# Performance work log

Measured on AMD Instinct MI355X. Metric: run time of the kernel, lower is better.

The kernel has to match this reference:

```python
import jax, jax.numpy as jnp
import numpy as np
from jax import lax

B, N, R, L = 16, 256, 24, 32
MEAN_STOP_TIME_S = 60.0
AVG_TRANSFER_WAIT_TIME_S = 300.0
SYMMETRIC_ROUTES = True
INF = jnp.inf


def setup_inputs() -> dict:
    key = jax.random.key(0)
    k1, k2, k3 = jax.random.split(key, 3)
    drive_times = jax.random.uniform(k1, (B, N, N), jnp.float32) * 1000.0 + 30.0
    demand = jax.random.uniform(k2, (B, N, N), jnp.float32) * 10.0
    demand = demand * (1.0 - jnp.eye(N, dtype=jnp.float32))  # no self-demand
    batch_routes = jax.random.randint(k3, (B, R, L), 0, N, dtype=jnp.int32)
    return {"drive_times": drive_times, "demand": demand, "batch_routes": batch_routes}


def _route_edges_and_legs(routes, dtm):
    # routes: [B,R,L] node ids (no -1 padding in this setup); dtm: [B,N,N]
    b = jnp.arange(B)[:, None, None]
    sf, st = routes[:, :, :-1], routes[:, :, 1:]
    leg_fwd = dtm[b, sf, st] + MEAN_STOP_TIME_S            # [B,R,L-1]
    zero = jnp.zeros((B, R, 1), dtm.dtype)
    cum_f = jnp.concatenate([zero, jnp.cumsum(leg_fwd, -1)], -1)  # [B,R,L]
    tri = jnp.triu(jnp.ones((L, L), dtype=bool), 1)
    # ride time from stop position i to position j>i along the route
    t_f = jnp.where(tri, cum_f[:, :, None, :] - cum_f[:, :, :, None], INF)
    b4 = jnp.arange(B)[:, None, None, None]
    src = jnp.broadcast_to(routes[:, :, :, None], (B, R, L, L))
    dst = jnp.broadcast_to(routes[:, :, None, :], (B, R, L, L))
    edge = jnp.full((B, N, N), INF, dtm.dtype)
    edge = edge.at[b4, src, dst].min(t_f)
    leg_rev = None
    if SYMMETRIC_ROUTES:
        leg_rev = dtm[b, st, sf] + MEAN_STOP_TIME_S        # reverse-direction legs
        cum_r = jnp.concatenate([zero, jnp.cumsum(leg_rev, -1)], -1)
        t_r = jnp.where(tri, cum_r[:, :, None, :] - cum_r[:, :, :, None], INF)
        edge = edge.at[b4, dst, src].min(t_r)              # ride from s_j back to s_i
    return edge, leg_fwd, leg_rev


def _floyd_warshall(edge):
    # batched FW, also tracking hop count of shortest paths
    idx = jnp.arange(N)
    dist = edge.at[:, idx, idx].set(0.0)
    offdiag = ~jnp.eye(N, dtype=bool)
    hops = jnp.where(jnp.isfinite(dist) & offdiag, 1.0, 0.0)

    def body(carry, k):
        d, h = carry
        dc = lax.dynamic_slice_in_dim(d, k, 1, axis=2)  # [B,N,1]
        dr = lax.dynamic_slice_in_dim(d, k, 1, axis=1)  # [B,1,N]
        hc = lax.dynamic_slice_in_dim(h, k, 1, axis=2)
        hr = lax.dynamic_slice_in_dim(h, k, 1, axis=1)
        alt = dc + dr
        better = alt < d
        return (jnp.where(better, alt, d), jnp.where(better, hc + hr, h)), None

    (dist, hops), _ = lax.scan(body, (dist, hops), idx)
    return dist, hops


def reference(drive_times, demand, batch_routes):
    edge, leg_fwd, leg_rev = _route_edges_and_legs(batch_routes, drive_times)
    dist, hops = _floyd_warshall(edge)
    nopath = jnp.isinf(dist)
    path_lens = jnp.where(nopath, 0.0, hops + 1.0)  # n nodes on path (diag -> 1)
    transfers = jnp.where(path_lens == 0.0, 0.0, path_lens - 2.0)
    trip_times = jnp.where(nopath, 0.0, dist + transfers * AVG_TRANSFER_WAIT_TIME_S)
    total_demand_time = (demand * trip_times).sum((1, 2))
    total_transfers = (demand * transfers).sum((1, 2))
    unserved_demand = jnp.where(nopath, demand, 0.0).sum((1, 2))
    total_demand = demand.sum((1, 2))
    n_disconnected = (nopath & (demand > 0)).sum((1, 2))
    buckets = [jnp.where(transfers == float(ii), demand, 0.0).sum((1, 2)) for ii in range(3)]
    d_un = jnp.where(transfers > 2.0, demand, 0.0).sum((1, 2)) + unserved_demand
    trips_at_transfers = jnp.stack(buckets + [d_un], axis=1)  # [B,4]
    total_route_time = leg_fwd.sum((1, 2))
    if SYMMETRIC_ROUTES:
        total_route_time = total_route_time + leg_rev.sum((1, 2))
    return (total_demand_time, total_route_time, trips_at_transfers,
            total_demand, unserved_demand, total_transfers, trip_times,
            n_disconnected)
```

## Files before the change

### kernel.cpp

```cpp
#include <hip/hip_runtime.h>

#define BB 16
#define NL 256
#define RR 24
#define LL 32
#define NN (NL*NL)
#define BNN (BB*NN)
#define TT 64

#define O_TDT 0
#define O_RT  16
#define O_TAT 32
#define O_TD  96
#define O_UNS 112
#define O_TTR 128
#define O_TT  144
#define O_ND  1048720

#define HSC 9.3132257461547852e-10
#define H2  1073741824.0
#define HMASK 8191

#define RIDX(r, c2) (((r)<<6) + ((((c2) ^ ((r)&31)))<<1))
#define LDD(A, r, c2) (*(double2*)&A[RIDX((r),(c2))])

__global__ void k_routes(const float* __restrict__ dtm, const int* __restrict__ routes,
                         unsigned long long* __restrict__ dist, float* __restrict__ acc){
    int br = blockIdx.x; int b = br / RR, r = br % RR;
    int lane = threadIdx.x;
    int gid = br*64 + lane;
    if (gid < BB*NL){
        int bq = gid >> 8, n = gid & 255;
        ((double*)dist)[bq*NN + n*(NL+1)] = 0.0;
    }
    __shared__ int   s[LL];
    __shared__ float lf[LL], lr[LL], cf[LL], cr[LL];
    if (lane < LL) s[lane] = routes[(b*RR + r)*LL + lane];
    __syncthreads();
    if (lane < LL-1){
        int a0 = s[lane], a1 = s[lane+1];
        const float* dt = dtm + b*NN;
        lf[lane] = dt[a0*NL + a1] + 60.0f;
        lr[lane] = dt[a1*NL + a0] + 60.0f;
    }
    __syncthreads();
    if (lane == 0){
        float af = 0.f, ar2 = 0.f;
        cf[0] = 0.f; cr[0] = 0.f;
        for (int l = 0; l < LL-1; l++){
            af += lf[l]; ar2 += lr[l];
            cf[l+1] = af; cr[l+1] = ar2;
        }
        atomicAdd(&acc[b*16 + 1], af + ar2);
    }
    __syncthreads();
    for (int p = lane; p < LL*LL; p += 64){
        int i = p >> 5, j = p & 31;
        if (j > i){
            double vf = (double)(cf[j] - cf[i]) + HSC;
            double vr = (double)(cr[j] - cr[i]) + HSC;
            atomicMin(&dist[b*NN + s[i]*NL + s[j]], (unsigned long long)__double_as_longlong(vf));
            atomicMin(&dist[b*NN + s[j]*NL + s[i]], (unsigned long long)__double_as_longlong(vr));
        }
    }
}

template<bool FINAL>
__global__ __launch_bounds__(512, 2) void k_fw(
        const double* __restrict__ src, double* __restrict__ dst, int kb,
        const float* __restrict__ demand, float* __restrict__ out,
        float* __restrict__ acc){
    int b  = blockIdx.y;
    int m  = blockIdx.x;
    int ti = m >> 2, tj = m & 3;
    int t  = threadIdx.x;
    int w  = t >> 6, lane = t & 63;
    int kh = lane >> 5, sub = lane & 31;
    int cA = sub & 15, cB = cA + 16;
    int r0 = w*8 + (sub >> 4)*4;
    __shared__ __align__(16) double KD[4096];
    __shared__ __align__(16) double BD[4096];
    const double* Kg = src + b*NN + kb*TT*(NL+1);
    const double* Bg = src + b*NN + (kb*NL + tj)*TT;
    const double* Cg = src + b*NN + (ti*NL + kb)*TT;
    const double* Dg = src + b*NN + (ti*NL + tj)*TT;

    double2 c0r[4];
    #pragma unroll
    for (int u = 0; u < 4; u++){
        int fid = u*512 + t, row = fid >> 5, cc = fid & 31;
        c0r[u] = *(const double2*)(Cg + row*NL + cc*2);
    }
    double2 d0a[4], d0b[4];
    #pragma unroll
    for (int i = 0; i < 4; i++){
        d0a[i] = *(const double2*)(Dg + (r0+i)*NL + 2*cA);
        d0b[i] = *(const double2*)(Dg + (r0+i)*NL + 2*cB);
    }

    #pragma unroll
    for (int u = 0; u < 4; u++){
        int fid = u*512 + t, row = fid >> 5, cc = fid & 31;
        LDD(KD, row, cc) = *(const double2*)(Kg + row*NL + cc*2);
        LDD(BD, row, cc) = *(const double2*)(Bg + row*NL + cc*2);
    }
    __syncthreads();

    for (int skb = 0; skb < 4; skb++){
        int s0 = skb*16, sc2 = skb*8;
        if (t < 64){
            int i = t >> 2, jg = t & 3, rr = s0 + i, cbk = sc2 + jg*2;
            double2 m0 = LDD(KD, rr, cbk), m1 = LDD(KD, rr, cbk+1);
            double md4[4] = {m0.x, m0.y, m1.x, m1.y};
            #pragma unroll
            for (int k = 0; k < 16; k++){
                double rd[4];
                #pragma unroll
                for (int c = 0; c < 4; c++) rd[c] = __shfl(md4[c], (k<<2)|jg);
                double cd = __shfl(md4[k&3], (i<<2)|(k>>2));
                #pragma unroll
                for (int c = 0; c < 4; c++) md4[c] = fmin(md4[c], cd + rd[c]);
            }
            LDD(KD, rr, cbk)   = make_double2(md4[0], md4[1]);
            LDD(KD, rr, cbk+1) = make_double2(md4[2], md4[3]);
        }
        __syncthreads();
        {
            double sv[4], av[16];
            int pr, pcA, pcB;
            if (t < 256){ pr = s0 + (t >> 4); pcA = t & 15;            pcB = pcA + 16; }
            else        { int t2 = t - 256; pr = t2 >> 2; pcA = sc2 + (t2 & 3); pcB = pcA + 4; }
            double2 v0 = LDD(KD, pr, pcA), v1 = LDD(KD, pr, pcB);
            sv[0]=v0.x; sv[1]=v0.y; sv[2]=v1.x; sv[3]=v1.y;
            #pragma unroll
            for (int c = 0; c < 8; c++){
                double2 a2 = LDD(KD, pr, sc2 + c);
                av[2*c] = a2.x; av[2*c+1] = a2.y;
            }
            #pragma unroll
            for (int k = 0; k < 16; k++){
                double2 b0 = LDD(KD, s0+k, pcA), b1 = LDD(KD, s0+k, pcB);
                sv[0] = fmin(sv[0], av[k] + b0.x);
                sv[1] = fmin(sv[1], av[k] + b0.y);
                sv[2] = fmin(sv[2], av[k] + b1.x);
                sv[3] = fmin(sv[3], av[k] + b1.y);
            }
            __syncthreads();
            LDD(KD, pr, pcA) = make_double2(sv[0], sv[1]);
            LDD(KD, pr, pcB) = make_double2(sv[2], sv[3]);
        }
        __syncthreads();
        double dd[4][4];
        #pragma unroll
        for (int i = 0; i < 4; i++){
            double2 v0 = LDD(KD, r0+i, cA), v1 = LDD(KD, r0+i, cB);
            dd[i][0]=v0.x; dd[i][1]=v0.y; dd[i][2]=v1.x; dd[i][3]=v1.y;
        }
        #pragma unroll
        for (int q4 = 0; q4 < 2; q4++){
            int kc = sc2 + kh*4 + q4*2;
            int kr = s0 + kh*8 + q4*4;
            double a[4][4], bm[4][4];
            #pragma unroll
            for (int i = 0; i < 4; i++){
                double2 a0 = LDD(KD, r0+i, kc), a1 = LDD(KD, r0+i, kc+1);
                a[i][0]=a0.x; a[i][1]=a0.y; a[i][2]=a1.x; a[i][3]=a1.y;
            }
            #pragma unroll
            for (int q = 0; q < 4; q++){
                double2 b0 = LDD(KD, kr+q, cA), b1 = LDD(KD, kr+q, cB);
                bm[q][0]=b0.x; bm[q][1]=b0.y; bm[q][2]=b1.x; bm[q][3]=b1.y;
            }
            #pragma unroll
            for (int q = 0; q < 4; q++)
            #pragma unroll
            for (int i = 0; i < 4; i++)
            #pragma unroll
            for (int j = 0; j < 4; j++)
                dd[i][j] = fmin(dd[i][j], a[i][q] + bm[q][j]);
        }
        #pragma unroll
        for (int i = 0; i < 4; i++)
        #pragma unroll
        for (int j = 0; j < 4; j++)
            dd[i][j] = fmin(dd[i][j], __shfl_xor(dd[i][j], 32));
        __syncthreads();
        #pragma unroll
        for (int i = 0; i < 4; i++){
            LDD(KD, r0+i, cA) = make_double2(dd[i][0], dd[i][1]);
            LDD(KD, r0+i, cB) = make_double2(dd[i][2], dd[i][3]);
        }
        __syncthreads();
    }

    double nanv = __longlong_as_double(0x7FF07FF07FF07FF0LL);
    double md[4][4];
    #pragma unroll
    for (int i = 0; i < 4; i++)
    #pragma unroll
    for (int j = 0; j < 4; j++) md[i][j] = nanv;
    #pragma unroll 2
    for (int q4 = 0; q4 < 8; q4++){
        int kc = kh*16 + q4*2;
        int kr = kh*32 + q4*4;
        double a[4][4], bm[4][4];
        #pragma unroll
        for (int i = 0; i < 4; i++){
            double2 a0 = LDD(KD, r0+i, kc), a1 = LDD(KD, r0+i, kc+1);
            a[i][0]=a0.x; a[i][1]=a0.y; a[i][2]=a1.x; a[i][3]=a1.y;
        }
        #pragma unroll
        for (int q = 0; q < 4; q++){
            double2 b0 = LDD(BD, kr+q, cA), b1 = LDD(BD, kr+q, cB);
            bm[q][0]=b0.x; bm[q][1]=b0.y; bm[q][2]=b1.x; bm[q][3]=b1.y;
        }
        #pragma unroll
        for (int q = 0; q < 4; q++)
        #pragma unroll
        for (int i = 0; i < 4; i++)
        #pragma unroll
        for (int j = 0; j < 4; j++)
            md[i][j] = fmin(md[i][j], a[i][q] + bm[q][j]);
    }
    #pragma unroll
    for (int i = 0; i < 4; i++)
    #pragma unroll
    for (int j = 0; j < 4; j++)
        md[i][j] = fmin(md[i][j], __shfl_xor(md[i][j], 32));
    __syncthreads();
    #pragma unroll
    for (int i = 0; i < 4; i++){
        LDD(BD, r0+i, cA) = make_double2(md[i][0], md[i][1]);
        LDD(BD, r0+i, cB) = make_double2(md[i][2], md[i][3]);
    }
    #pragma unroll
    for (int u = 0; u < 4; u++){
        int fid = u*512 + t, row = fid >> 5, cc = fid & 31;
        LDD(KD, row, cc) = c0r[u];
    }
    __syncthreads();

    double dd[4][4];
    #pragma unroll
    for (int i = 0; i < 4; i++){
        dd[i][0]=d0a[i].x; dd[i][1]=d0a[i].y; dd[i][2]=d0b[i].x; dd[i][3]=d0b[i].y;
    }
    #pragma unroll 2
    for (int q4 = 0; q4 < 8; q4++){
        int kc = kh*16 + q4*2;
        int kr = kh*32 + q4*4;
        double a[4][4], bm[4][4];
        #pragma unroll
        for (int i = 0; i < 4; i++){
            double2 a0 = LDD(KD, r0+i, kc), a1 = LDD(KD, r0+i, kc+1);
            a[i][0]=a0.x; a[i][1]=a0.y; a[i][2]=a1.x; a[i][3]=a1.y;
        }
        #pragma unroll
        for (int q = 0; q < 4; q++){
            double2 b0 = LDD(BD, kr+q, cA), b1 = LDD(BD, kr+q, cB);
            bm[q][0]=b0.x; bm[q][1]=b0.y; bm[q][2]=b1.x; bm[q][3]=b1.y;
        }
        #pragma unroll
        for (int q = 0; q < 4; q++)
        #pragma unroll
        for (int i = 0; i < 4; i++)
        #pragma unroll
        for (int j = 0; j < 4; j++)
            dd[i][j] = fmin(dd[i][j], a[i][q] + bm[q][j]);
    }
    #pragma unroll
    for (int i = 0; i < 4; i++)
    #pragma unroll
    for (int j = 0; j < 4; j++)
        dd[i][j] = fmin(dd[i][j], __shfl_xor(dd[i][j], 32));

    if (!FINAL){
        if (kh == 0){
            double* Od = dst + b*NN + (ti*NL + tj)*TT;
            #pragma unroll
            for (int i = 0; i < 4; i++){
                *(double2*)(Od + (r0+i)*NL + 2*cA) = make_double2(dd[i][0], dd[i][1]);
                *(double2*)(Od + (r0+i)*NL + 2*cB) = make_double2(dd[i][2], dd[i][3]);
            }
        }
        return;
    }

    float s9[9];
    #pragma unroll
    for (int q = 0; q < 9; q++) s9[q] = 0.f;
    if (kh == 0){
        #pragma unroll
        for (int i = 0; i < 4; i++){
            const float* dmg = demand + b*NN + (ti*TT + r0 + i)*NL + tj*TT;
            float* ttg = out + O_TT + b*NN + (ti*TT + r0 + i)*NL + tj*TT;
            float2 m0 = *(const float2*)(dmg + 2*cA);
            float2 m1 = *(const float2*)(dmg + 2*cB);
            float dmv[4] = {m0.x, m0.y, m1.x, m1.y};
            float tts[4];
            #pragma unroll
            for (int e = 0; e < 4; e++){
                double v = dd[i][e];
                bool np = !(v < 1e37);
                double vv = np ? 0.0 : v;
                int h = (int)(((long long)(vv * H2)) & (long long)HMASK);
                float d = (float)vv;
                float dm = dmv[e];
                float pl = np ? 0.f : (float)(h + 1);
                float tr = (pl == 0.f) ? 0.f : pl - 2.f;
                float tt = np ? 0.f : d + tr*300.f;
                tts[e] = tt;
                s9[0] += dm*tt;
                s9[1] += dm*tr;
                s9[2] += np ? dm : 0.f;
                s9[3] += dm;
                s9[4] += (np && dm > 0.f) ? 1.f : 0.f;
                s9[5] += (tr == 0.f) ? dm : 0.f;
                s9[6] += (tr == 1.f) ? dm : 0.f;
                s9[7] += (tr == 2.f) ? dm : 0.f;
                s9[8] += (tr > 2.f) ? dm : 0.f;
            }
            *(float2*)(ttg + 2*cA) = make_float2(tts[0], tts[1]);
            *(float2*)(ttg + 2*cB) = make_float2(tts[2], tts[3]);
        }
    }
    #define RED(x) { x += __shfl_down(x,32); x += __shfl_down(x,16); x += __shfl_down(x,8); \
                     x += __shfl_down(x,4);  x += __shfl_down(x,2);  x += __shfl_down(x,1); }
    #pragma unroll
    for (int q = 0; q < 9; q++) RED(s9[q])
    __syncthreads();
    float* red = (float*)KD;
    if (lane == 0){
        #pragma unroll
        for (int q = 0; q < 9; q++) red[w*9 + q] = s9[q];
    }
    __syncthreads();
    if (t < 9){
        float v = 0.f;
        #pragma unroll
        for (int ww = 0; ww < 8; ww++) v += red[ww*9 + t];
        int slot = (t == 0) ? 0 : t + 1;
        atomicAdd(&acc[b*16 + slot], v);
    }
    __syncthreads();
    __shared__ int isLast;
    if (t == 0){
        unsigned prev = atomicAdd((unsigned int*)(acc + 255), 1u);
        isLast = (prev == 255u) ? 1 : 0;
    }
    __syncthreads();
    if (isLast && t < BB){
        int bb = t;
        float a[10];
        #pragma unroll
        for (int s = 0; s < 10; s++) a[s] = atomicAdd(&acc[bb*16 + s], 0.f);
        out[O_TDT + bb] = a[0];
        out[O_RT  + bb] = a[1];
        out[O_TAT + 4*bb + 0] = a[6];
        out[O_TAT + 4*bb + 1] = a[7];
        out[O_TAT + 4*bb + 2] = a[8];
        out[O_TAT + 4*bb + 3] = a[9] + a[3];
        out[O_TD  + bb] = a[4];
        out[O_UNS + bb] = a[3];
        out[O_TTR + bb] = a[2];
        out[O_ND  + bb] = a[5];
    }
}

extern "C" void kernel_launch(void* const* d_in, const int* in_sizes, int n_in,
                              void* d_out, int out_size, void* d_ws, size_t ws_size,
                              hipStream_t stream){
    (void)in_sizes; (void)n_in; (void)out_size; (void)ws_size;
    const float* dtm    = (const float*)d_in[0];
    const float* demand = (const float*)d_in[1];
    const int*   routes = (const int*)d_in[2];
    float* out = (float*)d_out;
    double* distA = (double*)d_ws;
    double* distB = distA + BNN;
    float*  acc   = (float*)(distB + BNN);

    hipMemsetD32Async((hipDeviceptr_t)distA, 0x7FF07FF0u, (size_t)BNN*2, stream);
    hipMemsetAsync(acc, 0, 256*sizeof(float), stream);
    k_routes<<<BB*RR, 64, 0, stream>>>(dtm, routes, (unsigned long long*)distA, acc);
    k_fw<false><<<dim3(16,BB), 512, 0, stream>>>(distA, distB, 0, nullptr, nullptr, nullptr);
    k_fw<false><<<dim3(16,BB), 512, 0, stream>>>(distB, distA, 1, nullptr, nullptr, nullptr);
    k_fw<false><<<dim3(16,BB), 512, 0, stream>>>(distA, distB, 2, nullptr, nullptr, nullptr);
    k_fw<true> <<<dim3(16,BB), 512, 0, stream>>>(distB, nullptr, 3, demand, out, acc);
}
```

Measured before the change: 251.6 us.

## Remap FW tile threads to 2x4 outputs each, drop k-split shuffle reduction

Each thread now owns a 2x4 block of outputs over the full k range. Previously the k dimension was split across two half-waves, which needed a shuffle-xor min-reduction and left half the lanes idle during stores and the final epilogue. Removing the split cuts per-thread register tiles and lets all threads do useful store and epilogue work with wider float4 accesses. In exchange the serial k loop per thread is longer, the occupancy hint in launch_bounds is removed, and the new LDS access patterns may cause different bank conflicts.

```diff
diff --git a/kernel.cpp b/kernel.cpp
--- a/kernel.cpp
+++ b/kernel.cpp
@@ -66,7 +66,7 @@
 }
 
 template<bool FINAL>
-__global__ __launch_bounds__(512, 2) void k_fw(
+__global__ __launch_bounds__(512) void k_fw(
         const double* __restrict__ src, double* __restrict__ dst, int kb,
         const float* __restrict__ demand, float* __restrict__ out,
         float* __restrict__ acc){
@@ -74,10 +74,9 @@
     int m  = blockIdx.x;
     int ti = m >> 2, tj = m & 3;
     int t  = threadIdx.x;
-    int w  = t >> 6, lane = t & 63;
-    int kh = lane >> 5, sub = lane & 31;
-    int cA = sub & 15, cB = cA + 16;
-    int r0 = w*8 + (sub >> 4)*4;
+    int rp  = (t >> 4) * 2;
+    int cch = t & 15;
+    int c04 = cch * 4;
     __shared__ __align__(16) double KD[4096];
     __shared__ __align__(16) double BD[4096];
     const double* Kg = src + b*NN + kb*TT*(NL+1);
@@ -91,11 +90,11 @@
         int fid = u*512 + t, row = fid >> 5, cc = fid & 31;
         c0r[u] = *(const double2*)(Cg + row*NL + cc*2);
     }
-    double2 d0a[4], d0b[4];
-    #pragma unroll
-    for (int i = 0; i < 4; i++){
-        d0a[i] = *(const double2*)(Dg + (r0+i)*NL + 2*cA);
-        d0b[i] = *(const double2*)(Dg + (r0+i)*NL + 2*cB);
+    double2 d0a[2], d0b[2];
+    #pragma unroll
+    for (int i = 0; i < 2; i++){
+        d0a[i] = *(const double2*)(Dg + (rp+i)*NL + c04);
+        d0b[i] = *(const double2*)(Dg + (rp+i)*NL + c04 + 2);
     }
 
     #pragma unroll
@@ -150,88 +149,76 @@
             LDD(KD, pr, pcB) = make_double2(sv[2], sv[3]);
         }
         __syncthreads();
-        double dd[4][4];
-        #pragma unroll
-        for (int i = 0; i < 4; i++){
-            double2 v0 = LDD(KD, r0+i, cA), v1 = LDD(KD, r0+i, cB);
+        double dd[2][4];
+        #pragma unroll
+        for (int i = 0; i < 2; i++){
+            double2 v0 = LDD(KD, rp+i, cch*2), v1 = LDD(KD, rp+i, cch*2+1);
             dd[i][0]=v0.x; dd[i][1]=v0.y; dd[i][2]=v1.x; dd[i][3]=v1.y;
         }
         #pragma unroll
-        for (int q4 = 0; q4 < 2; q4++){
-            int kc = sc2 + kh*4 + q4*2;
-            int kr = s0 + kh*8 + q4*4;
-            double a[4][4], bm[4][4];
-            #pragma unroll
-            for (int i = 0; i < 4; i++){
-                double2 a0 = LDD(KD, r0+i, kc), a1 = LDD(KD, r0+i, kc+1);
+        for (int q4 = 0; q4 < 4; q4++){
+            int kr = s0 + q4*4;
+            double a[2][4], bm[4][4];
+            #pragma unroll
+            for (int i = 0; i < 2; i++){
+                double2 a0 = LDD(KD, rp+i, sc2+q4*2), a1 = LDD(KD, rp+i, sc2+q4*2+1);
                 a[i][0]=a0.x; a[i][1]=a0.y; a[i][2]=a1.x; a[i][3]=a1.y;
             }
             #pragma unroll
             for (int q = 0; q < 4; q++){
-                double2 b0 = LDD(KD, kr+q, cA), b1 = LDD(KD, kr+q, cB);
+                double2 b0 = LDD(KD, kr+q, cch*2), b1 = LDD(KD, kr+q, cch*2+1);
                 bm[q][0]=b0.x; bm[q][1]=b0.y; bm[q][2]=b1.x; bm[q][3]=b1.y;
             }
             #pragma unroll
             for (int q = 0; q < 4; q++)
             #pragma unroll
-            for (int i = 0; i < 4; i++)
+            for (int i = 0; i < 2; i++)
             #pragma unroll
             for (int j = 0; j < 4; j++)
                 dd[i][j] = fmin(dd[i][j], a[i][q] + bm[q][j]);
         }
-        #pragma unroll
-        for (int i = 0; i < 4; i++)
-        #pragma unroll
-        for (int j = 0; j < 4; j++)
-            dd[i][j] = fmin(dd[i][j], __shfl_xor(dd[i][j], 32));
         __syncthreads();
         #pragma unroll
-        for (int i = 0; i < 4; i++){
-            LDD(KD, r0+i, cA) = make_double2(dd[i][0], dd[i][1]);
-            LDD(KD, r0+i, cB) = make_double2(dd[i][2], dd[i][3]);
+        for (int i = 0; i < 2; i++){
+            LDD(KD, rp+i, cch*2)   = make_double2(dd[i][0], dd[i][1]);
+            LDD(KD, rp+i, cch*2+1) = make_double2(dd[i][2], dd[i][3]);
         }
         __syncthreads();
     }
 
     double nanv = __longlong_as_double(0x7FF07FF07FF07FF0LL);
-    double md[4][4];
-    #pragma unroll
-    for (int i = 0; i < 4; i++)
+    double md[2][4];
+    #pragma unroll
+    for (int i = 0; i < 2; i++)
     #pragma unroll
     for (int j = 0; j < 4; j++) md[i][j] = nanv;
-    #pragma unroll 2
-    for (int q4 = 0; q4 < 8; q4++){
-        int kc = kh*16 + q4*2;
-        int kr = kh*32 + q4*4;
-        double a[4][4], bm[4][4];
-        #pragma unroll
-        for (int i = 0; i < 4; i++){
-            double2 a0 = LDD(KD, r0+i, kc), a1 = LDD(KD, r0+i, kc+1);
+    #pragma unroll 4
+    for (int q4 = 0; q4 < 16; q4++){
+        int kr = q4*4;
+        double a[2][4], bm[4][4];
+        #pragma unroll
+        for (int i = 0; i < 2; i++){
+            double2 a0 = LDD(KD, rp+i, q4*2), a1 = LDD(KD, rp+i, q4*2+1);
             a[i][0]=a0.x; a[i][1]=a0.y; a[i][2]=a1.x; a[i][3]=a1.y;
         }
         #pragma unroll
         for (int q = 0; q < 4; q++){
-            double2 b0 = LDD(BD, kr+q, cA), b1 = LDD(BD, kr+q, cB);
+            double2 b0 = LDD(BD, kr+q, cch*2), b1 = LDD(BD, kr+q, cch*2+1);
             bm[q][0]=b0.x; bm[q][1]=b0.y; bm[q][2]=b1.x; bm[q][3]=b1.y;
         }
         #pragma unroll
         for (int q = 0; q < 4; q++)
         #pragma unroll
-        for (int i = 0; i < 4; i++)
+        for (int i = 0; i < 2; i++)
         #pragma unroll
         for (int j = 0; j < 4; j++)
             md[i][j] = fmin(md[i][j], a[i][q] + bm[q][j]);
     }
-    #pragma unroll
-    for (int i = 0; i < 4; i++)
-    #pragma unroll
-    for (int j = 0; j < 4; j++)
-        md[i][j] = fmin(md[i][j], __shfl_xor(md[i][j], 32));
-    __syncthreads();
-    #pragma unroll
-    for (int i = 0; i < 4; i++){
-        LDD(BD, r0+i, cA) = make_double2(md[i][0], md[i][1]);
-        LDD(BD, r0+i, cB) = make_double2(md[i][2], md[i][3]);
+    __syncthreads();
+    #pragma unroll
+    for (int i = 0; i < 2; i++){
+        LDD(BD, rp+i, cch*2)   = make_double2(md[i][0], md[i][1]);
+        LDD(BD, rp+i, cch*2+1) = make_double2(md[i][2], md[i][3]);
     }
     #pragma unroll
     for (int u = 0; u < 4; u++){
@@ -240,48 +227,40 @@
     }
     __syncthreads();
 
-    double dd[4][4];
-    #pragma unroll
-    for (int i = 0; i < 4; i++){
+    double dd[2][4];
+    #pragma unroll
+    for (int i = 0; i < 2; i++){
         dd[i][0]=d0a[i].x; dd[i][1]=d0a[i].y; dd[i][2]=d0b[i].x; dd[i][3]=d0b[i].y;
     }
-    #pragma unroll 2
-    for (int q4 = 0; q4 < 8; q4++){
-        int kc = kh*16 + q4*2;
-        int kr = kh*32 + q4*4;
-        double a[4][4], bm[4][4];
-        #pragma unroll
-        for (int i = 0; i < 4; i++){
-            double2 a0 = LDD(KD, r0+i, kc), a1 = LDD(KD, r0+i, kc+1);
+    #pragma unroll 4
+    for (int q4 = 0; q4 < 16; q4++){
+        int kr = q4*4;
+        double a[2][4], bm[4][4];
+        #pragma unroll
+        for (int i = 0; i < 2; i++){
+            double2 a0 = LDD(KD, rp+i, q4*2), a1 = LDD(KD, rp+i, q4*2+1);
             a[i][0]=a0.x; a[i][1]=a0.y; a[i][2]=a1.x; a[i][3]=a1.y;
         }
         #pragma unroll
         for (int q = 0; q < 4; q++){
-            double2 b0 = LDD(BD, kr+q, cA), b1 = LDD(BD, kr+q, cB);
+            double2 b0 = LDD(BD, kr+q, cch*2), b1 = LDD(BD, kr+q, cch*2+1);
             bm[q][0]=b0.x; bm[q][1]=b0.y; bm[q][2]=b1.x; bm[q][3]=b1.y;
         }
         #pragma unroll
         for (int q = 0; q < 4; q++)
         #pragma unroll
-        for (int i = 0; i < 4; i++)
+        for (int i = 0; i < 2; i++)
         #pragma unroll
         for (int j = 0; j < 4; j++)
             dd[i][j] = fmin(dd[i][j], a[i][q] + bm[q][j]);
     }
-    #pragma unroll
-    for (int i = 0; i < 4; i++)
-    #pragma unroll
-    for (int j = 0; j < 4; j++)
-        dd[i][j] = fmin(dd[i][j], __shfl_xor(dd[i][j], 32));
 
     if (!FINAL){
-        if (kh == 0){
-            double* Od = dst + b*NN + (ti*NL + tj)*TT;
-            #pragma unroll
-            for (int i = 0; i < 4; i++){
-                *(double2*)(Od + (r0+i)*NL + 2*cA) = make_double2(dd[i][0], dd[i][1]);
-                *(double2*)(Od + (r0+i)*NL + 2*cB) = make_double2(dd[i][2], dd[i][3]);
-            }
+        double* Od = dst + b*NN + (ti*NL + tj)*TT;
+        #pragma unroll
+        for (int i = 0; i < 2; i++){
+            *(double2*)(Od + (rp+i)*NL + c04)     = make_double2(dd[i][0], dd[i][1]);
+            *(double2*)(Od + (rp+i)*NL + c04 + 2) = make_double2(dd[i][2], dd[i][3]);
         }
         return;
     }
@@ -289,40 +268,36 @@
     float s9[9];
     #pragma unroll
     for (int q = 0; q < 9; q++) s9[q] = 0.f;
-    if (kh == 0){
-        #pragma unroll
-        for (int i = 0; i < 4; i++){
-            const float* dmg = demand + b*NN + (ti*TT + r0 + i)*NL + tj*TT;
-            float* ttg = out + O_TT + b*NN + (ti*TT + r0 + i)*NL + tj*TT;
-            float2 m0 = *(const float2*)(dmg + 2*cA);
-            float2 m1 = *(const float2*)(dmg + 2*cB);
-            float dmv[4] = {m0.x, m0.y, m1.x, m1.y};
-            float tts[4];
-            #pragma unroll
-            for (int e = 0; e < 4; e++){
-                double v = dd[i][e];
-                bool np = !(v < 1e37);
-                double vv = np ? 0.0 : v;
-                int h = (int)(((long long)(vv * H2)) & (long long)HMASK);
-                float d = (float)vv;
-                float dm = dmv[e];
-                float pl = np ? 0.f : (float)(h + 1);
-                float tr = (pl == 0.f) ? 0.f : pl - 2.f;
-                float tt = np ? 0.f : d + tr*300.f;
-                tts[e] = tt;
-                s9[0] += dm*tt;
-                s9[1] += dm*tr;
-                s9[2] += np ? dm : 0.f;
-                s9[3] += dm;
-                s9[4] += (np && dm > 0.f) ? 1.f : 0.f;
-                s9[5] += (tr == 0.f) ? dm : 0.f;
-                s9[6] += (tr == 1.f) ? dm : 0.f;
-                s9[7] += (tr == 2.f) ? dm : 0.f;
-                s9[8] += (tr > 2.f) ? dm : 0.f;
-            }
-            *(float2*)(ttg + 2*cA) = make_float2(tts[0], tts[1]);
-            *(float2*)(ttg + 2*cB) = make_float2(tts[2], tts[3]);
-        }
+    #pragma unroll
+    for (int i = 0; i < 2; i++){
+        const float* dmg = demand + b*NN + (ti*TT + rp + i)*NL + tj*TT;
+        float* ttg = out + O_TT + b*NN + (ti*TT + rp + i)*NL + tj*TT;
+        float4 mv = *(const float4*)(dmg + c04);
+        float dmv[4] = {mv.x, mv.y, mv.z, mv.w};
+        float tts[4];
+        #pragma unroll
+        for (int e = 0; e < 4; e++){
+            double v = dd[i][e];
+            bool np = !(v < 1e37);
+            double vv = np ? 0.0 : v;
+            int h = (int)(((long long)(vv * H2)) & (long long)HMASK);
+            float d = (float)vv;
+            float dm = dmv[e];
+            float pl = np ? 0.f : (float)(h + 1);
+            float tr = (pl == 0.f) ? 0.f : pl - 2.f;
+            float tt = np ? 0.f : d + tr*300.f;
+            tts[e] = tt;
+            s9[0] += dm*tt;
+            s9[1] += dm*tr;
+            s9[2] += np ? dm : 0.f;
+            s9[3] += dm;
+            s9[4] += (np && dm > 0.f) ? 1.f : 0.f;
+            s9[5] += (tr == 0.f) ? dm : 0.f;
+            s9[6] += (tr == 1.f) ? dm : 0.f;
+            s9[7] += (tr == 2.f) ? dm : 0.f;
+            s9[8] += (tr > 2.f) ? dm : 0.f;
+        }
+        *(float4*)(ttg + c04) = make_float4(tts[0], tts[1], tts[2], tts[3]);
     }
     #define RED(x) { x += __shfl_down(x,32); x += __shfl_down(x,16); x += __shfl_down(x,8); \
                      x += __shfl_down(x,4);  x += __shfl_down(x,2);  x += __shfl_down(x,1); }
@@ -330,6 +305,7 @@
     for (int q = 0; q < 9; q++) RED(s9[q])
     __syncthreads();
     float* red = (float*)KD;
+    int w = t >> 6, lane = t & 63;
     if (lane == 0){
         #pragma unroll
         for (int q = 0; q < 9; q++) red[w*9 + q] = s9[q];
```

Result: faster. 239.4 us (-4.8%).
